# Kernel tuning notes

Measured on AMD Instinct MI355X. Metric: run time of the kernel, lower is better.

## Reference

```python
import jax, jax.numpy as jnp
import numpy as np

H = 384          # hidden_dim == filter_size == n_chans
N_BINS = 256
PRED_GRAD = 0.1
LN_EPS = 1e-5


def _conv1d_same(x_bct, w_oik, b):
    k = w_oik.shape[-1]
    p = (k - 1) // 2
    y = jax.lax.conv_general_dilated(
        x_bct, w_oik, window_strides=(1,), padding=[(p, p)],
        dimension_numbers=("NCT", "OIT", "NCT"))
    return y + b[None, :, None]


def _ln_last(x, g, b):  # LayerNorm over last dim
    m = jnp.mean(x, axis=-1, keepdims=True)
    v = jnp.var(x, axis=-1, keepdims=True)
    return (x - m) * jax.lax.rsqrt(v + LN_EPS) * g + b


def _ln_chan(x_bct, g, b):  # LayerNorm over channel dim (dim=1)
    m = jnp.mean(x_bct, axis=1, keepdims=True)
    v = jnp.var(x_bct, axis=1, keepdims=True)
    return (x_bct - m) * jax.lax.rsqrt(v + LN_EPS) * g[None, :, None] + b[None, :, None]


def _sin_pos(x0, dim):
    # fairseq SinusoidalPositionalEmbedding, padding_idx=0, applied to xs[...,0]
    mask = (x0 != 0).astype(jnp.int32)
    pos = jnp.cumsum(mask, axis=1) * mask                        # [B,T]
    half = dim // 2
    inv = jnp.exp(jnp.arange(half, dtype=jnp.float32) * (-(np.log(10000.0) / (half - 1))))
    ang = pos[..., None].astype(jnp.float32) * inv               # [B,T,half]
    pe = jnp.concatenate([jnp.sin(ang), jnp.cos(ang)], axis=-1)  # [B,T,dim]
    return jnp.where(pos[..., None] == 0, 0.0, pe)


def _duration_predictor(x, src_mask, w1, b1, g1, be1, w2, b2, g2, be2, lw, lb):
    h = _conv1d_same(jnp.swapaxes(x, 1, 2), w1, b1)
    h = _ln_last(jax.nn.relu(jnp.swapaxes(h, 1, 2)), g1, be1)
    h = _conv1d_same(jnp.swapaxes(h, 1, 2), w2, b2)
    h = _ln_last(jax.nn.relu(jnp.swapaxes(h, 1, 2)), g2, be2)
    out = (h @ lw + lb)[..., 0]                                  # [B,T]
    return jnp.where(src_mask, 0.0, out)


def _variance_predictor(x, cw, cb, g, b, lw, lb, alpha):
    pos = alpha * _sin_pos(x[..., 0], x.shape[-1])
    h = jnp.swapaxes(x + pos, 1, 2)                              # [B,C,T]
    for i in range(cw.shape[0]):
        h = _ln_chan(jax.nn.relu(_conv1d_same(h, cw[i], cb[i])), g[i], b[i])
    return jnp.swapaxes(h, 1, 2) @ lw + lb                       # [B,T,odim]


def _length_regulate(x, dur_int, max_len):
    B, T, _ = x.shape
    cum = jnp.cumsum(dur_int, axis=1)                            # [B,T]
    frames = jnp.arange(max_len)
    idx = jax.vmap(lambda c: jnp.searchsorted(c, frames, side="right"))(cum)
    idx = jnp.clip(idx, 0, T - 1)                                # [B,max_len]
    out = jnp.take_along_axis(x, idx[..., None], axis=1)         # [B,max_len,H]
    total = cum[:, -1]
    valid = frames[None, :] < total[:, None]
    out = jnp.where(valid[..., None], out, 0.0)
    mel_len = jnp.minimum(total, max_len)
    return out, mel_len


def setup_inputs() -> dict:
    key = jax.random.key(0)
    ks = iter(jax.random.split(key, 40))
    B, T = 32, 1024
    rnd = lambda s: 0.02 * jax.random.normal(next(ks), s, dtype=jnp.float32)
    inp = {
        "x": jax.random.normal(next(ks), (B, T, H), dtype=jnp.float32),
        "src_lens": jax.random.randint(next(ks), (B,), 0, T),
        "src_mask": jnp.zeros((B, T), dtype=bool),
        "max_len": 4096,
        # duration predictor (kernel=3)
        "dp_w1": rnd((H, H, 3)), "dp_b1": jnp.zeros((H,)),
        "dp_ln1_g": jnp.ones((H,)), "dp_ln1_b": jnp.zeros((H,)),
        "dp_w2": rnd((H, H, 3)), "dp_b2": jnp.zeros((H,)),
        "dp_ln2_g": jnp.ones((H,)), "dp_ln2_b": jnp.zeros((H,)),
        "dp_lw": rnd((H, 1)), "dp_lb": jnp.full((1,), 1.5),  # bias -> avg dur ~3.5
        # pitch predictor: 5 layers, kernel=5, odim=1 (use_uv=False)
        "pp_cw": rnd((5, H, H, 5)), "pp_cb": jnp.zeros((5, H)),
        "pp_g": jnp.ones((5, H)), "pp_b": jnp.zeros((5, H)),
        "pp_lw": rnd((H, 1)), "pp_lb": jnp.zeros((1,)), "pp_alpha": jnp.ones((1,)),
        # energy predictor: 2 layers, kernel=5, odim=1
        "ep_cw": rnd((2, H, H, 5)), "ep_cb": jnp.zeros((2, H)),
        "ep_g": jnp.ones((2, H)), "ep_b": jnp.zeros((2, H)),
        "ep_lw": rnd((H, 1)), "ep_lb": jnp.zeros((1,)), "ep_alpha": jnp.ones((1,)),
        # bins (requires_grad=False buffers) + embedding tables
        "pitch_bins": jnp.linspace(-4.0, 4.0, N_BINS - 1),
        "energy_bins": jnp.linspace(-4.0, 4.0, N_BINS - 1),
        "pitch_table": rnd((N_BINS, H)),
        "energy_table": rnd((N_BINS, H)),
    }
    return inp


def reference(x, src_lens, src_mask, max_len,
              dp_w1, dp_b1, dp_ln1_g, dp_ln1_b, dp_w2, dp_b2, dp_ln2_g, dp_ln2_b, dp_lw, dp_lb,
              pp_cw, pp_cb, pp_g, pp_b, pp_lw, pp_lb, pp_alpha,
              ep_cw, ep_cb, ep_g, ep_b, ep_lw, ep_lb, ep_alpha,
              pitch_bins, energy_bins, pitch_table, energy_table):
    # duration (inference path: no targets, controls = 1.0)
    log_d = _duration_predictor(x, src_mask, dp_w1, dp_b1, dp_ln1_g, dp_ln1_b,
                                dp_w2, dp_b2, dp_ln2_g, dp_ln2_b, dp_lw, dp_lb)
    dur = jnp.clip(jnp.round(jnp.exp(log_d) - 1.0), 0.0, None)
    dur_int = dur.astype(jnp.int32)

    # straight-through-style grad scaling on predictor inputs
    xg = jax.lax.stop_gradient(x) + PRED_GRAD * (x - jax.lax.stop_gradient(x))

    # phoneme-level pitch (use_uv=False -> squeeze, bucketize)
    pitch_pred = _variance_predictor(xg, pp_cw, pp_cb, pp_g, pp_b, pp_lw, pp_lb, pp_alpha)[..., 0]
    pitch_idx = jnp.searchsorted(pitch_bins, pitch_pred, side="left")  # torch.bucketize(right=False)
    pitch_emb = pitch_table[pitch_idx]

    # phoneme-level energy
    energy_pred = _variance_predictor(xg, ep_cw, ep_cb, ep_g, ep_b, ep_lw, ep_lb, ep_alpha)[..., 0]
    energy_idx = jnp.searchsorted(energy_bins, energy_pred, side="left")
    energy_emb = energy_table[energy_idx]

    x_adapt = x + pitch_emb + energy_emb
    out, mel_len = _length_regulate(x_adapt, dur_int, int(max_len))
    return out, log_d, dur, pitch_pred, energy_pred, mel_len
```

## Files before the change

### kernel.cpp

```cpp
#include <hip/hip_runtime.h>
#include <cstdint>

#define HH 384
#define NBINS 256

typedef __attribute__((ext_vector_type(8))) short short8v;
typedef __attribute__((ext_vector_type(16))) float f32x16;
typedef __attribute__((ext_vector_type(4))) unsigned short ushort4v;

__device__ inline float4 ld4(const float* p){ return *(const float4*)p; }

__device__ inline unsigned short bf16_rne(float f){
  unsigned u = __float_as_uint(f);
  unsigned r = u + 0x7FFFu + ((u >> 16) & 1u);
  return (unsigned short)(r >> 16);
}
__device__ inline float bf16_to_f(unsigned short h){
  return __uint_as_float(((unsigned)h) << 16);
}

__global__ __launch_bounds__(1024) void pos_kernel(const float* __restrict__ x,
    int* __restrict__ pos, int T)
{
  __shared__ int s[1024];
  int b = blockIdx.x, tid = threadIdx.x;
  int m = 0;
  if (tid < T) m = (x[((size_t)b*T + tid)*HH] != 0.f) ? 1 : 0;
  s[tid] = m;
  __syncthreads();
  for (int off = 1; off < 1024; off <<= 1){
    int add = (tid >= off) ? s[tid-off] : 0;
    __syncthreads();
    s[tid] += add;
    __syncthreads();
  }
  if (tid < T) pos[(size_t)b*T + tid] = s[tid] * m;
}

__global__ __launch_bounds__(HH) void add_pe_kernel(const float* __restrict__ x,
    const int* __restrict__ pos, const float* __restrict__ alpha,
    float* __restrict__ out)
{
  int row = blockIdx.x; int i = threadIdx.x;
  int p = pos[row];
  float pe = 0.f;
  if (p != 0){
    int j = (i < HH/2) ? i : i - HH/2;
    float inv = expf((float)j * -0.04822167734018944f);
    float ang = (float)p * inv;
    pe = (i < HH/2) ? sinf(ang) : cosf(ang);
  }
  out[(size_t)row*HH + i] = x[(size_t)row*HH + i] + alpha[0]*pe;
}

template<int K>
__global__ __launch_bounds__(256) void wtrans_kernel(const float* __restrict__ w,
    unsigned short* __restrict__ dst, int nlayers)
{
  constexpr int SPL = (24*K + 2) * 6144;
  const int per = 384*384;
  int gid = blockIdx.x*256 + threadIdx.x;
  if (gid >= nlayers*per) return;
  int l = gid / per, rem = gid - l*per;
  int o = rem / 384, i = rem - (rem/384)*384;
  unsigned short* whi = dst + (size_t)l*2*SPL;
  unsigned short* wlo = whi + SPL;
  const float* wl = w + (size_t)l*384*384*K;
  int ph = (i >= 192) ? 1 : 0;
  int iloc = i - 192*ph;
  int c = iloc >> 4, half = (iloc >> 3) & 1, jj = iloc & 7;
  #pragma unroll
  for (int k = 0; k < K; ++k){
    float v = wl[((size_t)o*384 + i)*K + k];
    unsigned short hi = bf16_rne(v);
    unsigned short lo = bf16_rne(v - bf16_to_f(hi));
    int s = ph*12*K + k*12 + c;
    size_t d = ((size_t)(s*2 + half)*384 + o)*8 + jj;
    whi[d] = hi; wlo[d] = lo;
  }
}

template<int K>
__global__ __launch_bounds__(256) void conv_mfma_kernel(
    const float* __restrict__ in, const unsigned short* __restrict__ whi,
    const unsigned short* __restrict__ wlo, const float* __restrict__ bias,
    const float* __restrict__ g, const float* __restrict__ be,
    float* __restrict__ out, int T)
{
  constexpr int MT  = 32;
  constexpr int P   = (K-1)/2;
  constexpr int RT  = MT + K - 1;
  constexpr int RA  = RT + 2;
  constexpr int SPH = 12*K;
  constexpr int LDPc = 200;
  __shared__ unsigned short xs_hi[RA*LDPc];
  __shared__ unsigned short xs_lo[RA*LDPc];
  __shared__ float ps[4][32], pq[4][32];

  int ntile = T / MT;
  int b  = blockIdx.x / ntile;
  int t0 = (blockIdx.x % ntile) * MT;
  int tid = threadIdx.x;
  const float* inb = in + (size_t)b*T*HH;

  int wv = tid >> 6, ln = tid & 63;
  int l31 = ln & 31, hl = ln >> 5;
  int o0 = wv * 96;

  f32x16 acc[3];
  #pragma unroll
  for (int nt = 0; nt < 3; ++nt){
    float bv = bias[o0 + nt*32 + l31];
    #pragma unroll
    for (int r = 0; r < 16; ++r) acc[nt][r] = bv;
  }

  for (int phse = 0; phse < 2; ++phse){
    if (phse) __syncthreads();

    for (int e4 = tid; e4 < RT*48; e4 += 256){
      int r = e4 / 48, c4 = (e4 - r*48)*4;
      int t = t0 + r - P;
      float4 v = (t >= 0 && t < T) ? ld4(&inb[(size_t)t*HH + phse*192 + c4])
                                   : make_float4(0.f,0.f,0.f,0.f);
      float va[4] = {v.x, v.y, v.z, v.w};
      ushort4v h, l;
      #pragma unroll
      for (int q = 0; q < 4; ++q){
        unsigned short hq = bf16_rne(va[q]);
        h[q] = hq;
        l[q] = bf16_rne(va[q] - bf16_to_f(hq));
      }
      *(ushort4v*)&xs_hi[r*LDPc + c4] = h;
      *(ushort4v*)&xs_lo[r*LDPc + c4] = l;
    }
    __syncthreads();

    const unsigned short* bhp = whi + (size_t)phse*SPH*6144
                                    + ((size_t)hl*384 + o0 + l31)*8;
    const unsigned short* blp = wlo + (size_t)phse*SPH*6144
                                    + ((size_t)hl*384 + o0 + l31)*8;
    int aoff = l31*LDPc + hl*8;
    int cc = 0;

    short8v B0h[3], B0l[3], B1h[3], B1l[3], B2h[3], B2l[3];
    short8v A0h, A0l, A1h, A1l, A2h, A2l;

#define ADV do{ bhp += 6144; blp += 6144; aoff += 16;                        \
                if (++cc == 12){ cc = 0; aoff += LDPc - 192; } }while(0)

    #pragma unroll
    for (int nt = 0; nt < 3; ++nt){
      B0h[nt] = *(const short8v*)(bhp + nt*256);
      B0l[nt] = *(const short8v*)(blp + nt*256);
    }
    A0h = *(const short8v*)&xs_hi[aoff];
    A0l = *(const short8v*)&xs_lo[aoff];
    ADV;
    #pragma unroll
    for (int nt = 0; nt < 3; ++nt){
      B1h[nt] = *(const short8v*)(bhp + nt*256);
      B1l[nt] = *(const short8v*)(blp + nt*256);
    }
    A1h = *(const short8v*)&xs_hi[aoff];
    A1l = *(const short8v*)&xs_lo[aoff];
    ADV;

#define PHASE(NBh,NBl,NAh,NAl,CBh,CBl,CAh,CAl) do{                           \
    _Pragma("unroll")                                                        \
    for (int nt = 0; nt < 3; ++nt){                                          \
      NBh[nt] = *(const short8v*)(bhp + nt*256);                             \
      NBl[nt] = *(const short8v*)(blp + nt*256);                             \
    }                                                                        \
    NAh = *(const short8v*)&xs_hi[aoff];                                     \
    NAl = *(const short8v*)&xs_lo[aoff];                                     \
    ADV;                                                                     \
    __builtin_amdgcn_sched_barrier(0);                                       \
    __builtin_amdgcn_s_setprio(1);                                           \
    _Pragma("unroll")                                                        \
    for (int nt = 0; nt < 3; ++nt)                                           \
      acc[nt] = __builtin_amdgcn_mfma_f32_32x32x16_bf16(CAh, CBh[nt], acc[nt], 0,0,0); \
    _Pragma("unroll")                                                        \
    for (int nt = 0; nt < 3; ++nt)                                           \
      acc[nt] = __builtin_amdgcn_mfma_f32_32x32x16_bf16(CAh, CBl[nt], acc[nt], 0,0,0); \
    _Pragma("unroll")                                                        \
    for (int nt = 0; nt < 3; ++nt)                                           \
      acc[nt] = __builtin_amdgcn_mfma_f32_32x32x16_bf16(CAl, CBh[nt], acc[nt], 0,0,0); \
    __builtin_amdgcn_s_setprio(0);                                           \
  } while(0)

    for (int s = 0; s < SPH; s += 3){
      PHASE(B2h,B2l,A2h,A2l, B0h,B0l,A0h,A0l);
      PHASE(B0h,B0l,A0h,A0l, B1h,B1l,A1h,A1l);
      PHASE(B1h,B1l,A1h,A1l, B2h,B2l,A2h,A2l);
    }
#undef PHASE
#undef ADV
  }

  float gv[3], bev[3];
  #pragma unroll
  for (int nt = 0; nt < 3; ++nt){
    gv[nt]  = g[o0 + nt*32 + l31];
    bev[nt] = be[o0 + nt*32 + l31];
  }

  #pragma unroll
  for (int r = 0; r < 16; ++r){
    float s1 = 0.f, s2 = 0.f;
    #pragma unroll
    for (int nt = 0; nt < 3; ++nt){
      float v = fmaxf(acc[nt][r], 0.f);
      acc[nt][r] = v;
      s1 += v; s2 += v*v;
    }
    s1 += __shfl_xor(s1, 1);  s2 += __shfl_xor(s2, 1);
    s1 += __shfl_xor(s1, 2);  s2 += __shfl_xor(s2, 2);
    s1 += __shfl_xor(s1, 4);  s2 += __shfl_xor(s2, 4);
    s1 += __shfl_xor(s1, 8);  s2 += __shfl_xor(s2, 8);
    s1 += __shfl_xor(s1, 16); s2 += __shfl_xor(s2, 16);
    if (l31 == 0){
      int t = (r&3) + 8*(r>>2) + 4*hl;
      ps[wv][t] = s1; pq[wv][t] = s2;
    }
  }
  __syncthreads();

  #pragma unroll
  for (int r = 0; r < 16; ++r){
    int t = (r&3) + 8*(r>>2) + 4*hl;
    float s1 = ps[0][t] + ps[1][t] + ps[2][t] + ps[3][t];
    float s2 = pq[0][t] + pq[1][t] + pq[2][t] + pq[3][t];
    float mn  = s1 * (1.f/HH);
    float var = fmaxf(s2 * (1.f/HH) - mn*mn, 0.f);
    float rr  = rsqrtf(var + 1e-5f);
    float* orow = out + ((size_t)b*T + t0 + t)*HH;
    #pragma unroll
    for (int nt = 0; nt < 3; ++nt)
      orow[o0 + nt*32 + l31] = (acc[nt][r] - mn)*rr*gv[nt] + bev[nt];
  }
}

__global__ __launch_bounds__(256) void proj_var_kernel(const float* __restrict__ h,
    const float* __restrict__ lw, const float* __restrict__ lb,
    const float* __restrict__ bins, float* __restrict__ pred,
    int* __restrict__ idx, int nrows)
{
  int lane = threadIdx.x & 63, wid = threadIdx.x >> 6;
  int wave = blockIdx.x*4 + wid, nw = gridDim.x*4;
  float lwr[6];
  #pragma unroll
  for (int j = 0; j < 6; ++j) lwr[j] = lw[lane + 64*j];
  float lbv = lb[0];
  for (int row = wave; row < nrows; row += nw){
    const float* hr = h + (size_t)row*HH;
    float s = 0.f;
    #pragma unroll
    for (int j = 0; j < 6; ++j) s = fmaf(hr[lane + 64*j], lwr[j], s);
    #pragma unroll
    for (int off = 32; off; off >>= 1) s += __shfl_xor(s, off);
    if (lane == 0){
      float v = s + lbv;
      pred[row] = v;
      int lo = 0, hi = NBINS - 1;
      while (lo < hi){ int mid = (lo + hi) >> 1; if (bins[mid] < v) lo = mid + 1; else hi = mid; }
      idx[row] = lo;
    }
  }
}

__global__ __launch_bounds__(256) void proj_dur_kernel(const float* __restrict__ h,
    const float* __restrict__ lw, const float* __restrict__ lb,
    const unsigned char* __restrict__ mask, float* __restrict__ logd,
    float* __restrict__ durf, int* __restrict__ duri, int nrows)
{
  int lane = threadIdx.x & 63, wid = threadIdx.x >> 6;
  int wave = blockIdx.x*4 + wid, nw = gridDim.x*4;
  float lwr[6];
  #pragma unroll
  for (int j = 0; j < 6; ++j) lwr[j] = lw[lane + 64*j];
  float lbv = lb[0];
  for (int row = wave; row < nrows; row += nw){
    const float* hr = h + (size_t)row*HH;
    float s = 0.f;
    #pragma unroll
    for (int j = 0; j < 6; ++j) s = fmaf(hr[lane + 64*j], lwr[j], s);
    #pragma unroll
    for (int off = 32; off; off >>= 1) s += __shfl_xor(s, off);
    if (lane == 0){
      float v = s + lbv;
      if (mask[row]) v = 0.f;
      logd[row] = v;
      float d = fmaxf(rintf(expf(v) - 1.f), 0.f);
      durf[row] = d;
      duri[row] = (int)d;
    }
  }
}

__global__ __launch_bounds__(1024) void cumsum_kernel(const int* __restrict__ duri,
    int* __restrict__ cum, float* __restrict__ mel, int T, int ML)
{
  __shared__ int s[1024];
  int b = blockIdx.x, tid = threadIdx.x;
  s[tid] = (tid < T) ? duri[(size_t)b*T + tid] : 0;
  __syncthreads();
  for (int off = 1; off < 1024; off <<= 1){
    int add = (tid >= off) ? s[tid-off] : 0;
    __syncthreads();
    s[tid] += add;
    __syncthreads();
  }
  if (tid < T) cum[(size_t)b*T + tid] = s[tid];
  if (tid == T-1) mel[b] = (float)min(s[tid], ML);
}

__global__ __launch_bounds__(256) void xadapt_kernel(const float* __restrict__ x,
    const int* __restrict__ ip, const int* __restrict__ ie,
    const float* __restrict__ pt, const float* __restrict__ et,
    float* __restrict__ xa, int nrows)
{
  int gid = blockIdx.x*256 + threadIdx.x;
  int n4 = nrows * (HH/4);
  if (gid >= n4) return;
  int row = gid / (HH/4);
  int c = gid - row*(HH/4);
  float4 xv = ((const float4*)x)[gid];
  const float4* pr = (const float4*)(pt + (size_t)ip[row]*HH);
  const float4* er = (const float4*)(et + (size_t)ie[row]*HH);
  float4 pv = pr[c], ev = er[c];
  ((float4*)xa)[gid] = make_float4(xv.x+pv.x+ev.x, xv.y+pv.y+ev.y,
                                   xv.z+pv.z+ev.z, xv.w+pv.w+ev.w);
}

__global__ __launch_bounds__(256) void lr_kernel(const float* __restrict__ xa,
    const int* __restrict__ cum, float* __restrict__ out, int T, int ML)
{
  constexpr int FR = 32;
  __shared__ int scum[1024];
  __shared__ int sidx[FR];
  __shared__ int svalid[FR];
  int b  = blockIdx.y;
  int f0 = blockIdx.x * FR;
  for (int i = threadIdx.x; i < T; i += 256) scum[i] = cum[(size_t)b*T + i];
  __syncthreads();
  int total = scum[T-1];
  if (threadIdx.x < FR){
    int f = f0 + threadIdx.x;
    int lo = 0, hi = T;
    while (lo < hi){ int mid = (lo + hi) >> 1; if (scum[mid] <= f) lo = mid + 1; else hi = mid; }
    sidx[threadIdx.x] = min(lo, T-1);
    svalid[threadIdx.x] = (f < total) ? 1 : 0;
  }
  __syncthreads();
  #pragma unroll
  for (int it = 0; it < FR*(HH/4)/256; ++it){
    int item = it*256 + threadIdx.x;
    int fl = item / (HH/4);
    int c  = item - fl*(HH/4);
    int f  = f0 + fl;
    if (f >= ML) continue;
    float4 v = make_float4(0.f,0.f,0.f,0.f);
    if (svalid[fl]) v = ((const float4*)(xa + ((size_t)b*T + sidx[fl])*HH))[c];
    ((float4*)(out + ((size_t)b*ML + f)*HH))[c] = v;
  }
}

extern "C" void kernel_launch(void* const* d_in, const int* in_sizes, int n_in,
                              void* d_out, int out_size, void* d_ws, size_t ws_size,
                              hipStream_t stream)
{
  const float* x        = (const float*)d_in[0];
  const unsigned char* src_mask = (const unsigned char*)d_in[2];
  const float* dp_w1 = (const float*)d_in[4];
  const float* dp_b1 = (const float*)d_in[5];
  const float* dp_g1 = (const float*)d_in[6];
  const float* dp_be1= (const float*)d_in[7];
  const float* dp_w2 = (const float*)d_in[8];
  const float* dp_b2 = (const float*)d_in[9];
  const float* dp_g2 = (const float*)d_in[10];
  const float* dp_be2= (const float*)d_in[11];
  const float* dp_lw = (const float*)d_in[12];
  const float* dp_lb = (const float*)d_in[13];
  const float* pp_cw = (const float*)d_in[14];
  const float* pp_cb = (const float*)d_in[15];
  const float* pp_g  = (const float*)d_in[16];
  const float* pp_b  = (const float*)d_in[17];
  const float* pp_lw = (const float*)d_in[18];
  const float* pp_lb = (const float*)d_in[19];
  const float* pp_alpha = (const float*)d_in[20];
  const float* ep_cw = (const float*)d_in[21];
  const float* ep_cb = (const float*)d_in[22];
  const float* ep_g  = (const float*)d_in[23];
  const float* ep_b  = (const float*)d_in[24];
  const float* ep_lw = (const float*)d_in[25];
  const float* ep_lb = (const float*)d_in[26];
  const float* ep_alpha = (const float*)d_in[27];
  const float* pbins = (const float*)d_in[28];
  const float* ebins = (const float*)d_in[29];
  const float* ptab  = (const float*)d_in[30];
  const float* etab  = (const float*)d_in[31];

  int B = in_sizes[1];
  int T = in_sizes[0] / (B*HH);
  int ML = (int)(((long long)out_size - B - 4LL*B*T) / ((long long)B*HH));
  size_t rows = (size_t)B*T;

  float* bufA = (float*)d_ws;
  float* bufB = bufA + rows*HH;
  int* pos    = (int*)(bufB + rows*HH);
  int* idx_p  = pos + rows;
  int* idx_e  = idx_p + rows;
  int* dur_i  = idx_e + rows;
  int* cum    = dur_i + rows;

  float* out0    = (float*)d_out;
  float* logd    = out0 + (size_t)B*ML*HH;
  float* durf    = logd + rows;
  float* pitchp  = durf + rows;
  float* energyp = pitchp + rows;
  float* mel     = energyp + rows;

  const size_t SPL5 = (size_t)(24*5 + 2)*6144;
  const size_t SPL3 = (size_t)(24*3 + 2)*6144;
  unsigned short* wsc    = (unsigned short*)d_out;
  unsigned short* pitchW = wsc;
  unsigned short* enerW  = pitchW + 5*2*SPL5;
  unsigned short* durW1  = enerW  + 2*2*SPL5;
  unsigned short* durW2  = durW1  + 2*SPL3;

  const int per = 384*384;
  wtrans_kernel<5><<<(5*per + 255)/256, 256, 0, stream>>>(pp_cw, pitchW, 5);
  wtrans_kernel<5><<<(2*per + 255)/256, 256, 0, stream>>>(ep_cw, enerW, 2);
  wtrans_kernel<3><<<(per + 255)/256, 256, 0, stream>>>(dp_w1, durW1, 1);
  wtrans_kernel<3><<<(per + 255)/256, 256, 0, stream>>>(dp_w2, durW2, 1);

  int conv_grid = B * (T / 32);

  pos_kernel<<<B, 1024, 0, stream>>>(x, pos, T);

  add_pe_kernel<<<(int)rows, HH, 0, stream>>>(x, pos, pp_alpha, bufA);
  {
    float* src = bufA; float* dst = bufB;
    for (int l = 0; l < 5; ++l){
      unsigned short* whi = pitchW + (size_t)l*2*SPL5;
      conv_mfma_kernel<5><<<conv_grid, 256, 0, stream>>>(src, whi, whi + SPL5,
          pp_cb + (size_t)l*HH, pp_g + (size_t)l*HH, pp_b + (size_t)l*HH, dst, T);
      float* t2 = dst; dst = src; src = t2;
    }
    proj_var_kernel<<<256, 256, 0, stream>>>(src, pp_lw, pp_lb, pbins,
                                             pitchp, idx_p, (int)rows);
  }

  add_pe_kernel<<<(int)rows, HH, 0, stream>>>(x, pos, ep_alpha, bufA);
  {
    float* src = bufA; float* dst = bufB;
    for (int l = 0; l < 2; ++l){
      unsigned short* whi = enerW + (size_t)l*2*SPL5;
      conv_mfma_kernel<5><<<conv_grid, 256, 0, stream>>>(src, whi, whi + SPL5,
          ep_cb + (size_t)l*HH, ep_g + (size_t)l*HH, ep_b + (size_t)l*HH, dst, T);
      float* t2 = dst; dst = src; src = t2;
    }
    proj_var_kernel<<<256, 256, 0, stream>>>(src, ep_lw, ep_lb, ebins,
                                             energyp, idx_e, (int)rows);
  }

  conv_mfma_kernel<3><<<conv_grid, 256, 0, stream>>>(x, durW1, durW1 + SPL3,
      dp_b1, dp_g1, dp_be1, bufB, T);
  conv_mfma_kernel<3><<<conv_grid, 256, 0, stream>>>(bufB, durW2, durW2 + SPL3,
      dp_b2, dp_g2, dp_be2, bufA, T);
  proj_dur_kernel<<<256, 256, 0, stream>>>(bufA, dp_lw, dp_lb, src_mask,
                                           logd, durf, dur_i, (int)rows);

  cumsum_kernel<<<B, 1024, 0, stream>>>(dur_i, cum, mel, T, ML);

  xadapt_kernel<<<(int)((rows*(HH/4) + 255)/256), 256, 0, stream>>>(
      x, idx_p, idx_e, ptab, etab, bufB, (int)rows);

  lr_kernel<<<dim3(ML/32, B), 256, 0, stream>>>(bufB, cum, out0, T, ML);
}
```

Baseline: 1.615 ms.

## Double conv tile to 64 timesteps so each weight fragment feeds two MFMA tiles

Each conv block now covers 64 timesteps instead of 32. Every wave keeps two sets of accumulators, one per 32-row half, and reuses each hi/lo weight fragment loaded from global memory for both halves. This halves the weight traffic per output row, which was re-read by every block. The price is twice the accumulator registers, a shallower software pipeline (two stages instead of three), and half as many blocks in the grid, which may leave CUs less occupied.

```diff
diff --git a/kernel.cpp b/kernel.cpp
--- a/kernel.cpp
+++ b/kernel.cpp
@@ -87,7 +87,7 @@
     const float* __restrict__ g, const float* __restrict__ be,
     float* __restrict__ out, int T)
 {
-  constexpr int MT  = 32;
+  constexpr int MT  = 64;
   constexpr int P   = (K-1)/2;
   constexpr int RT  = MT + K - 1;
   constexpr int RA  = RT + 2;
@@ -95,7 +95,7 @@
   constexpr int LDPc = 200;
   __shared__ unsigned short xs_hi[RA*LDPc];
   __shared__ unsigned short xs_lo[RA*LDPc];
-  __shared__ float ps[4][32], pq[4][32];
+  __shared__ float ps[4][64], pq[4][64];
 
   int ntile = T / MT;
   int b  = blockIdx.x / ntile;
@@ -107,12 +107,12 @@
   int l31 = ln & 31, hl = ln >> 5;
   int o0 = wv * 96;
 
-  f32x16 acc[3];
+  f32x16 acc0[3], acc1[3];
   #pragma unroll
   for (int nt = 0; nt < 3; ++nt){
     float bv = bias[o0 + nt*32 + l31];
     #pragma unroll
-    for (int r = 0; r < 16; ++r) acc[nt][r] = bv;
+    for (int r = 0; r < 16; ++r){ acc0[nt][r] = bv; acc1[nt][r] = bv; }
   }
 
   for (int phse = 0; phse < 2; ++phse){
@@ -140,61 +140,65 @@
                                     + ((size_t)hl*384 + o0 + l31)*8;
     const unsigned short* blp = wlo + (size_t)phse*SPH*6144
                                     + ((size_t)hl*384 + o0 + l31)*8;
-    int aoff = l31*LDPc + hl*8;
+    int aoff0 = l31*LDPc + hl*8;
+    int aoff1 = (32 + l31)*LDPc + hl*8;
     int cc = 0;
 
-    short8v B0h[3], B0l[3], B1h[3], B1l[3], B2h[3], B2l[3];
-    short8v A0h, A0l, A1h, A1l, A2h, A2l;
-
-#define ADV do{ bhp += 6144; blp += 6144; aoff += 16;                        \
-                if (++cc == 12){ cc = 0; aoff += LDPc - 192; } }while(0)
+    short8v B0h[3], B0l[3], B1h[3], B1l[3];
+    short8v A00h, A00l, A01h, A01l;
+    short8v A10h, A10l, A11h, A11l;
+
+#define ADV do{ bhp += 6144; blp += 6144; aoff0 += 16; aoff1 += 16;          \
+                if (++cc == 12){ cc = 0; aoff0 += LDPc - 192;                \
+                                 aoff1 += LDPc - 192; } }while(0)
 
     #pragma unroll
     for (int nt = 0; nt < 3; ++nt){
       B0h[nt] = *(const short8v*)(bhp + nt*256);
       B0l[nt] = *(const short8v*)(blp + nt*256);
     }
-    A0h = *(const short8v*)&xs_hi[aoff];
-    A0l = *(const short8v*)&xs_lo[aoff];
+    A00h = *(const short8v*)&xs_hi[aoff0];
+    A00l = *(const short8v*)&xs_lo[aoff0];
+    A01h = *(const short8v*)&xs_hi[aoff1];
+    A01l = *(const short8v*)&xs_lo[aoff1];
     ADV;
-    #pragma unroll
-    for (int nt = 0; nt < 3; ++nt){
-      B1h[nt] = *(const short8v*)(bhp + nt*256);
-      B1l[nt] = *(const short8v*)(blp + nt*256);
-    }
-    A1h = *(const short8v*)&xs_hi[aoff];
-    A1l = *(const short8v*)&xs_lo[aoff];
-    ADV;
-
-#define PHASE(NBh,NBl,NAh,NAl,CBh,CBl,CAh,CAl) do{                           \
+
+#define STEP(NBh,NBl,NA0h,NA0l,NA1h,NA1l, CBh,CBl,CA0h,CA0l,CA1h,CA1l) do{   \
     _Pragma("unroll")                                                        \
     for (int nt = 0; nt < 3; ++nt){                                          \
       NBh[nt] = *(const short8v*)(bhp + nt*256);                             \
       NBl[nt] = *(const short8v*)(blp + nt*256);                             \
     }                                                                        \
-    NAh = *(const short8v*)&xs_hi[aoff];                                     \
-    NAl = *(const short8v*)&xs_lo[aoff];                                     \
+    NA0h = *(const short8v*)&xs_hi[aoff0];                                   \
+    NA0l = *(const short8v*)&xs_lo[aoff0];                                   \
+    NA1h = *(const short8v*)&xs_hi[aoff1];                                   \
+    NA1l = *(const short8v*)&xs_lo[aoff1];                                   \
     ADV;                                                                     \
     __builtin_amdgcn_sched_barrier(0);                                       \
     __builtin_amdgcn_s_setprio(1);                                           \
     _Pragma("unroll")                                                        \
-    for (int nt = 0; nt < 3; ++nt)                                           \
-      acc[nt] = __builtin_amdgcn_mfma_f32_32x32x16_bf16(CAh, CBh[nt], acc[nt], 0,0,0); \
+    for (int nt = 0; nt < 3; ++nt){                                          \
+      acc0[nt] = __builtin_amdgcn_mfma_f32_32x32x16_bf16(CA0h, CBh[nt], acc0[nt], 0,0,0); \
+      acc1[nt] = __builtin_amdgcn_mfma_f32_32x32x16_bf16(CA1h, CBh[nt], acc1[nt], 0,0,0); \
+    }                                                                        \
     _Pragma("unroll")                                                        \
-    for (int nt = 0; nt < 3; ++nt)                                           \
-      acc[nt] = __builtin_amdgcn_mfma_f32_32x32x16_bf16(CAh, CBl[nt], acc[nt], 0,0,0); \
+    for (int nt = 0; nt < 3; ++nt){                                          \
+      acc0[nt] = __builtin_amdgcn_mfma_f32_32x32x16_bf16(CA0h, CBl[nt], acc0[nt], 0,0,0); \
+      acc1[nt] = __builtin_amdgcn_mfma_f32_32x32x16_bf16(CA1h, CBl[nt], acc1[nt], 0,0,0); \
+    }                                                                        \
     _Pragma("unroll")                                                        \
-    for (int nt = 0; nt < 3; ++nt)                                           \
-      acc[nt] = __builtin_amdgcn_mfma_f32_32x32x16_bf16(CAl, CBh[nt], acc[nt], 0,0,0); \
+    for (int nt = 0; nt < 3; ++nt){                                          \
+      acc0[nt] = __builtin_amdgcn_mfma_f32_32x32x16_bf16(CA0l, CBh[nt], acc0[nt], 0,0,0); \
+      acc1[nt] = __builtin_amdgcn_mfma_f32_32x32x16_bf16(CA1l, CBh[nt], acc1[nt], 0,0,0); \
+    }                                                                        \
     __builtin_amdgcn_s_setprio(0);                                           \
   } while(0)
 
-    for (int s = 0; s < SPH; s += 3){
-      PHASE(B2h,B2l,A2h,A2l, B0h,B0l,A0h,A0l);
-      PHASE(B0h,B0l,A0h,A0l, B1h,B1l,A1h,A1l);
-      PHASE(B1h,B1l,A1h,A1l, B2h,B2l,A2h,A2l);
-    }
-#undef PHASE
+    for (int s = 0; s < SPH; s += 2){
+      STEP(B1h,B1l,A10h,A10l,A11h,A11l, B0h,B0l,A00h,A00l,A01h,A01l);
+      STEP(B0h,B0l,A00h,A00l,A01h,A01l, B1h,B1l,A10h,A10l,A11h,A11l);
+    }
+#undef STEP
 #undef ADV
   }
 
@@ -206,38 +210,46 @@
   }
 
   #pragma unroll
-  for (int r = 0; r < 16; ++r){
-    float s1 = 0.f, s2 = 0.f;
-    #pragma unroll
-    for (int nt = 0; nt < 3; ++nt){
-      float v = fmaxf(acc[nt][r], 0.f);
-      acc[nt][r] = v;
-      s1 += v; s2 += v*v;
-    }
-    s1 += __shfl_xor(s1, 1);  s2 += __shfl_xor(s2, 1);
-    s1 += __shfl_xor(s1, 2);  s2 += __shfl_xor(s2, 2);
-    s1 += __shfl_xor(s1, 4);  s2 += __shfl_xor(s2, 4);
-    s1 += __shfl_xor(s1, 8);  s2 += __shfl_xor(s2, 8);
-    s1 += __shfl_xor(s1, 16); s2 += __shfl_xor(s2, 16);
-    if (l31 == 0){
-      int t = (r&3) + 8*(r>>2) + 4*hl;
-      ps[wv][t] = s1; pq[wv][t] = s2;
+  for (int rg = 0; rg < 2; ++rg){
+    #pragma unroll
+    for (int r = 0; r < 16; ++r){
+      float s1 = 0.f, s2 = 0.f;
+      #pragma unroll
+      for (int nt = 0; nt < 3; ++nt){
+        float v = fmaxf(rg ? acc1[nt][r] : acc0[nt][r], 0.f);
+        if (rg) acc1[nt][r] = v; else acc0[nt][r] = v;
+        s1 += v; s2 += v*v;
+      }
+      s1 += __shfl_xor(s1, 1);  s2 += __shfl_xor(s2, 1);
+      s1 += __shfl_xor(s1, 2);  s2 += __shfl_xor(s2, 2);
+      s1 += __shfl_xor(s1, 4);  s2 += __shfl_xor(s2, 4);
+      s1 += __shfl_xor(s1, 8);  s2 += __shfl_xor(s2, 8);
+      s1 += __shfl_xor(s1, 16); s2 += __shfl_xor(s2, 16);
+      if (l31 == 0){
+        int t = rg*32 + (r&3) + 8*(r>>2) + 4*hl;
+        ps[wv][t] = s1; pq[wv][t] = s2;
+      }
     }
   }
   __syncthreads();
 
   #pragma unroll
-  for (int r = 0; r < 16; ++r){
-    int t = (r&3) + 8*(r>>2) + 4*hl;
-    float s1 = ps[0][t] + ps[1][t] + ps[2][t] + ps[3][t];
-    float s2 = pq[0][t] + pq[1][t] + pq[2][t] + pq[3][t];
-    float mn  = s1 * (1.f/HH);
-    float var = fmaxf(s2 * (1.f/HH) - mn*mn, 0.f);
-    float rr  = rsqrtf(var + 1e-5f);
-    float* orow = out + ((size_t)b*T + t0 + t)*HH;
-    #pragma unroll
-    for (int nt = 0; nt < 3; ++nt)
-      orow[o0 + nt*32 + l31] = (acc[nt][r] - mn)*rr*gv[nt] + bev[nt];
+  for (int rg = 0; rg < 2; ++rg){
+    #pragma unroll
+    for (int r = 0; r < 16; ++r){
+      int t = rg*32 + (r&3) + 8*(r>>2) + 4*hl;
+      float s1 = ps[0][t] + ps[1][t] + ps[2][t] + ps[3][t];
+      float s2 = pq[0][t] + pq[1][t] + pq[2][t] + pq[3][t];
+      float mn  = s1 * (1.f/HH);
+      float var = fmaxf(s2 * (1.f/HH) - mn*mn, 0.f);
+      float rr  = rsqrtf(var + 1e-5f);
+      float* orow = out + ((size_t)b*T + t0 + t)*HH;
+      #pragma unroll
+      for (int nt = 0; nt < 3; ++nt){
+        float v = rg ? acc1[nt][r] : acc0[nt][r];
+        orow[o0 + nt*32 + l31] = (v - mn)*rr*gv[nt] + bev[nt];
+      }
+    }
   }
 }
 
@@ -435,7 +447,7 @@
   wtrans_kernel<3><<<(per + 255)/256, 256, 0, stream>>>(dp_w1, durW1, 1);
   wtrans_kernel<3><<<(per + 255)/256, 256, 0, stream>>>(dp_w2, durW2, 1);
 
-  int conv_grid = B * (T / 32);
+  int conv_grid = B * (T / 64);
 
   pos_kernel<<<B, 1024, 0, stream>>>(x, pos, T);
 
```

Result: no change. 1.583 ms (-1.9%).

## Double conv time tile to 64 rows with 8 waves and asm-pipelined weight loads

Applied to the files above, without the earlier changes.

The conv kernel now handles 64 time rows per block with 512 threads. Each pair of row-group waves shares the same output-channel slice, so every weight fetch is amortised over twice as many rows, and the per-row LayerNorm partials are kept per row group. Weight loads are issued through inline asm global_load_dwordx4 with a manual s_waitcnt vmcnt and double buffering, replacing triple buffering, so they overlap with the MFMAs. The cost is half as many blocks, which lowers occupancy and parallelism at small B*T. Hand-placed waitcnt also relies on the compiler not reordering other memory operations around it.

```diff
diff --git a/kernel.cpp b/kernel.cpp
--- a/kernel.cpp
+++ b/kernel.cpp
@@ -81,13 +81,13 @@
 }
 
 template<int K>
-__global__ __launch_bounds__(256) void conv_mfma_kernel(
+__global__ __launch_bounds__(512) void conv_mfma_kernel(
     const float* __restrict__ in, const unsigned short* __restrict__ whi,
     const unsigned short* __restrict__ wlo, const float* __restrict__ bias,
     const float* __restrict__ g, const float* __restrict__ be,
     float* __restrict__ out, int T)
 {
-  constexpr int MT  = 32;
+  constexpr int MT  = 64;
   constexpr int P   = (K-1)/2;
   constexpr int RT  = MT + K - 1;
   constexpr int RA  = RT + 2;
@@ -95,7 +95,7 @@
   constexpr int LDPc = 200;
   __shared__ unsigned short xs_hi[RA*LDPc];
   __shared__ unsigned short xs_lo[RA*LDPc];
-  __shared__ float ps[4][32], pq[4][32];
+  __shared__ float ps[8][32], pq[8][32];
 
   int ntile = T / MT;
   int b  = blockIdx.x / ntile;
@@ -105,7 +105,8 @@
 
   int wv = tid >> 6, ln = tid & 63;
   int l31 = ln & 31, hl = ln >> 5;
-  int o0 = wv * 96;
+  int nw = wv & 3, rg = wv >> 2;
+  int o0 = nw * 96;
 
   f32x16 acc[3];
   #pragma unroll
@@ -115,10 +116,13 @@
     for (int r = 0; r < 16; ++r) acc[nt][r] = bv;
   }
 
+#define GLOAD(dst, p) \
+  asm volatile("global_load_dwordx4 %0, %1, off" : "=v"(dst) : "v"(p))
+
   for (int phse = 0; phse < 2; ++phse){
     if (phse) __syncthreads();
 
-    for (int e4 = tid; e4 < RT*48; e4 += 256){
+    for (int e4 = tid; e4 < RT*48; e4 += 512){
       int r = e4 / 48, c4 = (e4 - r*48)*4;
       int t = t0 + r - P;
       float4 v = (t >= 0 && t < T) ? ld4(&inb[(size_t)t*HH + phse*192 + c4])
@@ -140,41 +144,32 @@
                                     + ((size_t)hl*384 + o0 + l31)*8;
     const unsigned short* blp = wlo + (size_t)phse*SPH*6144
                                     + ((size_t)hl*384 + o0 + l31)*8;
-    int aoff = l31*LDPc + hl*8;
+    int aoff = (rg*32 + l31)*LDPc + hl*8;
     int cc = 0;
 
-    short8v B0h[3], B0l[3], B1h[3], B1l[3], B2h[3], B2l[3];
-    short8v A0h, A0l, A1h, A1l, A2h, A2l;
-
-#define ADV do{ bhp += 6144; blp += 6144; aoff += 16;                        \
-                if (++cc == 12){ cc = 0; aoff += LDPc - 192; } }while(0)
-
-    #pragma unroll
-    for (int nt = 0; nt < 3; ++nt){
-      B0h[nt] = *(const short8v*)(bhp + nt*256);
-      B0l[nt] = *(const short8v*)(blp + nt*256);
-    }
+    short8v B0h[3], B0l[3], B1h[3], B1l[3];
+    short8v A0h, A0l, A1h, A1l;
+
+#define ADVB do{ bhp += 6144; blp += 6144; }while(0)
+#define ADVA do{ aoff += 16;                                                 \
+                 if (++cc == 12){ cc = 0; aoff += LDPc - 192; } }while(0)
+
+    GLOAD(B0h[0], bhp);        GLOAD(B0h[1], bhp + 256); GLOAD(B0h[2], bhp + 512);
+    GLOAD(B0l[0], blp);        GLOAD(B0l[1], blp + 256); GLOAD(B0l[2], blp + 512);
+    ADVB;
     A0h = *(const short8v*)&xs_hi[aoff];
     A0l = *(const short8v*)&xs_lo[aoff];
-    ADV;
-    #pragma unroll
-    for (int nt = 0; nt < 3; ++nt){
-      B1h[nt] = *(const short8v*)(bhp + nt*256);
-      B1l[nt] = *(const short8v*)(blp + nt*256);
-    }
-    A1h = *(const short8v*)&xs_hi[aoff];
-    A1l = *(const short8v*)&xs_lo[aoff];
-    ADV;
-
-#define PHASE(NBh,NBl,NAh,NAl,CBh,CBl,CAh,CAl) do{                           \
-    _Pragma("unroll")                                                        \
-    for (int nt = 0; nt < 3; ++nt){                                          \
-      NBh[nt] = *(const short8v*)(bhp + nt*256);                             \
-      NBl[nt] = *(const short8v*)(blp + nt*256);                             \
-    }                                                                        \
+    ADVA;
+
+#define STEP(CBh,CBl,CAh,CAl, NBh,NBl,NAh,NAl) do{                           \
+    GLOAD(NBh[0], bhp);       GLOAD(NBh[1], bhp + 256);                      \
+    GLOAD(NBh[2], bhp + 512); GLOAD(NBl[0], blp);                            \
+    GLOAD(NBl[1], blp + 256); GLOAD(NBl[2], blp + 512);                      \
+    ADVB;                                                                    \
     NAh = *(const short8v*)&xs_hi[aoff];                                     \
     NAl = *(const short8v*)&xs_lo[aoff];                                     \
-    ADV;                                                                     \
+    ADVA;                                                                    \
+    asm volatile("s_waitcnt vmcnt(6)");                                      \
     __builtin_amdgcn_sched_barrier(0);                                       \
     __builtin_amdgcn_s_setprio(1);                                           \
     _Pragma("unroll")                                                        \
@@ -189,14 +184,18 @@
     __builtin_amdgcn_s_setprio(0);                                           \
   } while(0)
 
-    for (int s = 0; s < SPH; s += 3){
-      PHASE(B2h,B2l,A2h,A2l, B0h,B0l,A0h,A0l);
-      PHASE(B0h,B0l,A0h,A0l, B1h,B1l,A1h,A1l);
-      PHASE(B1h,B1l,A1h,A1l, B2h,B2l,A2h,A2l);
-    }
-#undef PHASE
-#undef ADV
-  }
+    for (int s = 0; s < SPH; s += 2){
+      STEP(B0h,B0l,A0h,A0l, B1h,B1l,A1h,A1l);
+      STEP(B1h,B1l,A1h,A1l, B0h,B0l,A0h,A0l);
+    }
+#undef STEP
+#undef ADVB
+#undef ADVA
+
+    asm volatile("s_waitcnt vmcnt(0)");
+    __builtin_amdgcn_sched_barrier(0);
+  }
+#undef GLOAD
 
   float gv[3], bev[3];
   #pragma unroll
@@ -229,12 +228,12 @@
   #pragma unroll
   for (int r = 0; r < 16; ++r){
     int t = (r&3) + 8*(r>>2) + 4*hl;
-    float s1 = ps[0][t] + ps[1][t] + ps[2][t] + ps[3][t];
-    float s2 = pq[0][t] + pq[1][t] + pq[2][t] + pq[3][t];
+    float s1 = ps[rg*4+0][t] + ps[rg*4+1][t] + ps[rg*4+2][t] + ps[rg*4+3][t];
+    float s2 = pq[rg*4+0][t] + pq[rg*4+1][t] + pq[rg*4+2][t] + pq[rg*4+3][t];
     float mn  = s1 * (1.f/HH);
     float var = fmaxf(s2 * (1.f/HH) - mn*mn, 0.f);
     float rr  = rsqrtf(var + 1e-5f);
-    float* orow = out + ((size_t)b*T + t0 + t)*HH;
+    float* orow = out + ((size_t)b*T + t0 + rg*32 + t)*HH;
     #pragma unroll
     for (int nt = 0; nt < 3; ++nt)
       orow[o0 + nt*32 + l31] = (acc[nt][r] - mn)*rr*gv[nt] + bev[nt];
@@ -435,7 +434,7 @@
   wtrans_kernel<3><<<(per + 255)/256, 256, 0, stream>>>(dp_w1, durW1, 1);
   wtrans_kernel<3><<<(per + 255)/256, 256, 0, stream>>>(dp_w2, durW2, 1);
 
-  int conv_grid = B * (T / 32);
+  int conv_grid = B * (T / 64);
 
   pos_kernel<<<B, 1024, 0, stream>>>(x, pos, T);
 
@@ -444,7 +443,7 @@
     float* src = bufA; float* dst = bufB;
     for (int l = 0; l < 5; ++l){
       unsigned short* whi = pitchW + (size_t)l*2*SPL5;
-      conv_mfma_kernel<5><<<conv_grid, 256, 0, stream>>>(src, whi, whi + SPL5,
+      conv_mfma_kernel<5><<<conv_grid, 512, 0, stream>>>(src, whi, whi + SPL5,
           pp_cb + (size_t)l*HH, pp_g + (size_t)l*HH, pp_b + (size_t)l*HH, dst, T);
       float* t2 = dst; dst = src; src = t2;
     }
@@ -457,7 +456,7 @@
     float* src = bufA; float* dst = bufB;
     for (int l = 0; l < 2; ++l){
       unsigned short* whi = enerW + (size_t)l*2*SPL5;
-      conv_mfma_kernel<5><<<conv_grid, 256, 0, stream>>>(src, whi, whi + SPL5,
+      conv_mfma_kernel<5><<<conv_grid, 512, 0, stream>>>(src, whi, whi + SPL5,
           ep_cb + (size_t)l*HH, ep_g + (size_t)l*HH, ep_b + (size_t)l*HH, dst, T);
       float* t2 = dst; dst = src; src = t2;
     }
@@ -465,9 +464,9 @@
                                              energyp, idx_e, (int)rows);
   }
 
-  conv_mfma_kernel<3><<<conv_grid, 256, 0, stream>>>(x, durW1, durW1 + SPL3,
+  conv_mfma_kernel<3><<<conv_grid, 512, 0, stream>>>(x, durW1, durW1 + SPL3,
       dp_b1, dp_g1, dp_be1, bufB, T);
-  conv_mfma_kernel<3><<<conv_grid, 256, 0, stream>>>(bufB, durW2, durW2 + SPL3,
+  conv_mfma_kernel<3><<<conv_grid, 512, 0, stream>>>(bufB, durW2, durW2 + SPL3,
       dp_b2, dp_g2, dp_be2, bufA, T);
   proj_dur_kernel<<<256, 256, 0, stream>>>(bufA, dp_lw, dp_lb, src_mask,
                                            logd, durf, dur_i, (int)rows);
```

Result: no change. 1.595 ms (-1.2%).
